# Performance work log

Hardware: AMD Instinct MI355X
Metric: run time of the kernel (lower is better)

## Reference

```python
import jax, jax.numpy as jnp
import numpy as np

EPS = 1e-8  # torch CosineSimilarity default eps

def _cosine(a, b):
    # cosine similarity along last dim, torch semantics: clamp norms to eps
    num = jnp.sum(a * b, axis=-1)
    na = jnp.maximum(jnp.linalg.norm(a, axis=-1), EPS)
    nb = jnp.maximum(jnp.linalg.norm(b, axis=-1), EPS)
    return num / (na * nb)

def setup_inputs() -> dict:
    key = jax.random.key(0)
    k1, k2, k3, k4, k5, k6 = jax.random.split(key, 6)
    B, D, NU, NS, K = 4096, 128, 100000, 50000, 5
    return {
        "user_embeddings": jax.random.normal(k1, (B, D), dtype=jnp.float32),
        "subreddit_embeddings": jax.random.normal(k2, (B, D), dtype=jnp.float32),
        "total_user_embeddings": jax.random.normal(k3, (NU, D), dtype=jnp.float32),
        "total_subreddit_embeddings": jax.random.normal(k4, (NS, D), dtype=jnp.float32),
        "batch_users": jax.random.randint(k5, (B,), 0, NU, dtype=jnp.int64) if jax.config.jax_enable_x64 else jax.random.randint(k5, (B,), 0, NU, dtype=jnp.int32),
        "neg_indices": jax.random.randint(k6, (B, K), 0, NS, dtype=jnp.int64) if jax.config.jax_enable_x64 else jax.random.randint(k6, (B, K), 0, NS, dtype=jnp.int32),
    }

def reference(user_embeddings, subreddit_embeddings, total_user_embeddings,
              total_subreddit_embeddings, batch_users, neg_indices):
    # positive term: cosine over paired batch embeddings
    pos = _cosine(user_embeddings, subreddit_embeddings)            # [B]
    # negative term: gather user table rows and sampled negative subreddit rows
    u = total_user_embeddings[batch_users]                          # [B, D]
    neg_emb = total_subreddit_embeddings[neg_indices]               # [B, K, D]
    neg = _cosine(u[:, None, :], neg_emb)                           # [B, K]
    positive_loss = 1.0 - jnp.mean(pos)
    negative_loss = jnp.mean(jnp.mean(neg, axis=-1))                # mean per user, then over users
    return positive_loss + negative_loss
```

## Files before the change

### kernel.cpp

```cpp
#include <hip/hip_runtime.h>
#include <math.h>

#define EPS 1e-8f
#define D 128
#define K 5

__global__ __launch_bounds__(256) void simloss_partial(
    const float* __restrict__ ue,
    const float* __restrict__ se,
    const float* __restrict__ tu,
    const float* __restrict__ ts,
    const int*   __restrict__ busers,
    const int*   __restrict__ negidx,
    float* __restrict__ partials,
    int B)
{
    const int t   = threadIdx.x;
    const int tid = blockIdx.x * 256 + t;
    const int row = tid >> 4;
    const int r   = t & 15;

    float diff = 0.0f;
    if (row < B) {
        const int uidx = busers[row];
        int nidx[K];
        #pragma unroll
        for (int k = 0; k < K; ++k) nidx[k] = negidx[row * K + k];

        const float4* A = (const float4*)(ue + (size_t)row * D);
        const float4* Bv = (const float4*)(se + (size_t)row * D);
        const float4 a0 = A[r],  a1 = A[r + 16];
        const float4 b0 = Bv[r], b1 = Bv[r + 16];
        float dot = a0.x*b0.x + a0.y*b0.y + a0.z*b0.z + a0.w*b0.w
                  + a1.x*b1.x + a1.y*b1.y + a1.z*b1.z + a1.w*b1.w;
        float na  = a0.x*a0.x + a0.y*a0.y + a0.z*a0.z + a0.w*a0.w
                  + a1.x*a1.x + a1.y*a1.y + a1.z*a1.z + a1.w*a1.w;
        float nb  = b0.x*b0.x + b0.y*b0.y + b0.z*b0.z + b0.w*b0.w
                  + b1.x*b1.x + b1.y*b1.y + b1.z*b1.z + b1.w*b1.w;

        const float4* Cv = (const float4*)(tu + (size_t)uidx * D);
        const float4 c0 = Cv[r], c1 = Cv[r + 16];
        float nc = c0.x*c0.x + c0.y*c0.y + c0.z*c0.z + c0.w*c0.w
                 + c1.x*c1.x + c1.y*c1.y + c1.z*c1.z + c1.w*c1.w;

        float dk[K], nk[K];
        #pragma unroll
        for (int k = 0; k < K; ++k) {
            const float4* E = (const float4*)(ts + (size_t)nidx[k] * D);
            const float4 e0 = E[r], e1 = E[r + 16];
            dk[k] = c0.x*e0.x + c0.y*e0.y + c0.z*e0.z + c0.w*e0.w
                  + c1.x*e1.x + c1.y*e1.y + c1.z*e1.z + c1.w*e1.w;
            nk[k] = e0.x*e0.x + e0.y*e0.y + e0.z*e0.z + e0.w*e0.w
                  + e1.x*e1.x + e1.y*e1.y + e1.z*e1.z + e1.w*e1.w;
        }

        #pragma unroll
        for (int off = 8; off > 0; off >>= 1) {
            dot += __shfl_xor(dot, off);
            na  += __shfl_xor(na,  off);
            nb  += __shfl_xor(nb,  off);
            nc  += __shfl_xor(nc,  off);
            #pragma unroll
            for (int k = 0; k < K; ++k) {
                dk[k] += __shfl_xor(dk[k], off);
                nk[k] += __shfl_xor(nk[k], off);
            }
        }

        const float pos = dot * rsqrtf(fmaxf(na, EPS * EPS))
                              * rsqrtf(fmaxf(nb, EPS * EPS));
        const float rc  = rsqrtf(fmaxf(nc, EPS * EPS));
        float s = 0.0f;
        #pragma unroll
        for (int k = 0; k < K; ++k)
            s += dk[k] * rc * rsqrtf(fmaxf(nk[k], EPS * EPS));
        diff = s * (1.0f / K) - pos;
    }

    __shared__ float sp[16];
    if (r == 0) sp[t >> 4] = diff;
    __syncthreads();
    if (t == 0) {
        float bp = 0.0f;
        #pragma unroll
        for (int i = 0; i < 16; ++i) bp += sp[i];
        partials[blockIdx.x] = bp;
    }
}

__global__ __launch_bounds__(64) void simloss_final(
    const float* __restrict__ partials, float* __restrict__ out, float invB)
{
    const int t = threadIdx.x;
    const float4 v = ((const float4*)partials)[t];
    float s = v.x + v.y + v.z + v.w;
    #pragma unroll
    for (int off = 32; off > 0; off >>= 1) s += __shfl_xor(s, off);
    if (t == 0) out[0] = 1.0f + s * invB;
}

extern "C" void kernel_launch(void* const* d_in, const int* in_sizes, int n_in,
                              void* d_out, int out_size, void* d_ws, size_t ws_size,
                              hipStream_t stream) {
    const float* ue = (const float*)d_in[0];
    const float* se = (const float*)d_in[1];
    const float* tu = (const float*)d_in[2];
    const float* ts = (const float*)d_in[3];
    const int*   bu = (const int*)d_in[4];
    const int*   ni = (const int*)d_in[5];
    float* out = (float*)d_out;

    const int B = in_sizes[0] / D;
    const int nblk = (B * 16 + 255) / 256;
    float* partials = (float*)d_ws;

    simloss_partial<<<nblk, 256, 0, stream>>>(ue, se, tu, ts, bu, ni, partials, B);
    simloss_final<<<1, 64, 0, stream>>>(partials, out, 1.0f / (float)B);
}
```

Before: 11.19 us.

## Fuse final reduction into main kernel via hierarchical atomic last-block counters

Replaces the two-kernel reduction with a single kernel in which each block publishes its partial sum and increments a two-level set of padded atomic counters. The block that finishes last sums all partials and writes the output, removing the second launch and its launch gap. The counters live in workspace and are never reset; they rely on wrapping modular arithmetic to detect the last block across calls. That works only when the workspace is zeroed initially and nblk is exactly 256, and it adds atomic and fence traffic to every block.

```diff
diff --git a/kernel.cpp b/kernel.cpp
--- a/kernel.cpp
+++ b/kernel.cpp
@@ -4,19 +4,25 @@
 #define EPS 1e-8f
 #define D 128
 #define K 5
+#define NG 16
+#define CPAD 16
 
-__global__ __launch_bounds__(256) void simloss_partial(
+__global__ __launch_bounds__(256) void simloss_onepass(
     const float* __restrict__ ue,
     const float* __restrict__ se,
     const float* __restrict__ tu,
     const float* __restrict__ ts,
     const int*   __restrict__ busers,
     const int*   __restrict__ negidx,
-    float* __restrict__ partials,
-    int B)
+    float*       __restrict__ out,
+    float*       __restrict__ partials,
+    unsigned*    __restrict__ cnt1,
+    unsigned*    __restrict__ cnt2,
+    int B, float invB, int nblk)
 {
+    const int bid = blockIdx.x;
     const int t   = threadIdx.x;
-    const int tid = blockIdx.x * 256 + t;
+    const int tid = bid * 256 + t;
     const int row = tid >> 4;
     const int r   = t & 15;
 
@@ -27,7 +33,7 @@
         #pragma unroll
         for (int k = 0; k < K; ++k) nidx[k] = negidx[row * K + k];
 
-        const float4* A = (const float4*)(ue + (size_t)row * D);
+        const float4* A  = (const float4*)(ue + (size_t)row * D);
         const float4* Bv = (const float4*)(se + (size_t)row * D);
         const float4 a0 = A[r],  a1 = A[r + 16];
         const float4 b0 = Bv[r], b1 = Bv[r + 16];
@@ -78,25 +84,64 @@
     }
 
     __shared__ float sp[16];
+    __shared__ int win;
     if (r == 0) sp[t >> 4] = diff;
     __syncthreads();
+
     if (t == 0) {
         float bp = 0.0f;
         #pragma unroll
         for (int i = 0; i < 16; ++i) bp += sp[i];
-        partials[blockIdx.x] = bp;
+        __hip_atomic_store((unsigned*)&partials[bid],
+                           __builtin_bit_cast(unsigned, bp),
+                           __ATOMIC_RELAXED, __HIP_MEMORY_SCOPE_AGENT);
+        __threadfence();
+        const int g = bid & (NG - 1);
+        int w2 = 0;
+        const unsigned o1 = __hip_atomic_fetch_add(&cnt1[g * CPAD], 1u,
+                               __ATOMIC_ACQ_REL, __HIP_MEMORY_SCOPE_AGENT);
+        if (((o1 + 1u) & (unsigned)(nblk / NG - 1)) == 0u) {
+            const unsigned o2 = __hip_atomic_fetch_add(cnt2, 1u,
+                                   __ATOMIC_ACQ_REL, __HIP_MEMORY_SCOPE_AGENT);
+            w2 = (((o2 + 1u) & (NG - 1)) == 0u);
+        }
+        win = w2;
     }
+    __syncthreads();
+    if (!win) return;
+
+    __threadfence();
+    float s = 0.0f;
+    if (t < nblk) {
+        const unsigned u = __hip_atomic_load((unsigned*)&partials[t],
+                              __ATOMIC_RELAXED, __HIP_MEMORY_SCOPE_AGENT);
+        s = __builtin_bit_cast(float, u);
+    }
+    #pragma unroll
+    for (int off = 32; off > 0; off >>= 1) s += __shfl_xor(s, off);
+
+    __shared__ float lw[4];
+    const int lane = t & 63, wave = t >> 6;
+    if (lane == 0) lw[wave] = s;
+    __syncthreads();
+    if (t == 0)
+        out[0] = 1.0f + (lw[0] + lw[1] + lw[2] + lw[3]) * invB;
 }
 
-__global__ __launch_bounds__(64) void simloss_final(
-    const float* __restrict__ partials, float* __restrict__ out, float invB)
+__global__ __launch_bounds__(256) void simloss_final(
+    const float* __restrict__ partials, float* __restrict__ out,
+    int nblk, float invB)
 {
     const int t = threadIdx.x;
-    const float4 v = ((const float4*)partials)[t];
-    float s = v.x + v.y + v.z + v.w;
+    float s = 0.0f;
+    for (int i = t; i < nblk; i += 256) s += partials[i];
     #pragma unroll
     for (int off = 32; off > 0; off >>= 1) s += __shfl_xor(s, off);
-    if (t == 0) out[0] = 1.0f + s * invB;
+    __shared__ float lw[4];
+    const int lane = t & 63, wave = t >> 6;
+    if (lane == 0) lw[wave] = s;
+    __syncthreads();
+    if (t == 0) out[0] = 1.0f + (lw[0] + lw[1] + lw[2] + lw[3]) * invB;
 }
 
 extern "C" void kernel_launch(void* const* d_in, const int* in_sizes, int n_in,
@@ -112,8 +157,19 @@
 
     const int B = in_sizes[0] / D;
     const int nblk = (B * 16 + 255) / 256;
-    float* partials = (float*)d_ws;
 
-    simloss_partial<<<nblk, 256, 0, stream>>>(ue, se, tu, ts, bu, ni, partials, B);
-    simloss_final<<<1, 64, 0, stream>>>(partials, out, 1.0f / (float)B);
+    float*    partials = (float*)d_ws;
+    unsigned* cnt1     = (unsigned*)(partials + nblk);
+    unsigned* cnt2     = cnt1 + NG * CPAD;
+
+    if (nblk == 256) {
+        simloss_onepass<<<nblk, 256, 0, stream>>>(ue, se, tu, ts, bu, ni, out,
+                                                  partials, cnt1, cnt2,
+                                                  B, 1.0f / (float)B, nblk);
+    } else {
+        simloss_onepass<<<nblk, 256, 0, stream>>>(ue, se, tu, ts, bu, ni, out,
+                                                  partials, cnt1, cnt2,
+                                                  B, 1.0f / (float)B, nblk);
+        simloss_final<<<1, 256, 0, stream>>>(partials, out, nblk, 1.0f / (float)B);
+    }
 }
```

Result: slower. 16.76 us (+49.8%).

## Fuse partial and final reduction into one cooperative kernel with grid sync

Applied to the files above, without the earlier changes.

Merges the two-kernel reduction into a single cooperative launch. Each block publishes its partial sum with an atomic store, then a grid-wide sync lets block 0 sum the 256 partials and write the result. This removes the second kernel launch and its inter-kernel gap, but adds the cost of a grid barrier and the cooperative launch path, which may be more expensive than a normal launch.

```diff
diff --git a/kernel.cpp b/kernel.cpp
--- a/kernel.cpp
+++ b/kernel.cpp
@@ -1,22 +1,27 @@
 #include <hip/hip_runtime.h>
+#include <hip/hip_cooperative_groups.h>
 #include <math.h>
+
+namespace cg = cooperative_groups;
 
 #define EPS 1e-8f
 #define D 128
 #define K 5
 
-__global__ __launch_bounds__(256) void simloss_partial(
+__global__ __launch_bounds__(256) void simloss_coop(
     const float* __restrict__ ue,
     const float* __restrict__ se,
     const float* __restrict__ tu,
     const float* __restrict__ ts,
     const int*   __restrict__ busers,
     const int*   __restrict__ negidx,
-    float* __restrict__ partials,
-    int B)
+    float*       __restrict__ out,
+    float*       __restrict__ partials,
+    int B, float invB)
 {
+    const int bid = blockIdx.x;
     const int t   = threadIdx.x;
-    const int tid = blockIdx.x * 256 + t;
+    const int tid = bid * 256 + t;
     const int row = tid >> 4;
     const int r   = t & 15;
 
@@ -27,7 +32,7 @@
         #pragma unroll
         for (int k = 0; k < K; ++k) nidx[k] = negidx[row * K + k];
 
-        const float4* A = (const float4*)(ue + (size_t)row * D);
+        const float4* A  = (const float4*)(ue + (size_t)row * D);
         const float4* Bv = (const float4*)(se + (size_t)row * D);
         const float4 a0 = A[r],  a1 = A[r + 16];
         const float4 b0 = Bv[r], b1 = Bv[r + 16];
@@ -84,19 +89,30 @@
         float bp = 0.0f;
         #pragma unroll
         for (int i = 0; i < 16; ++i) bp += sp[i];
-        partials[blockIdx.x] = bp;
+        __hip_atomic_store((unsigned*)&partials[bid],
+                           __builtin_bit_cast(unsigned, bp),
+                           __ATOMIC_RELAXED, __HIP_MEMORY_SCOPE_AGENT);
     }
-}
 
-__global__ __launch_bounds__(64) void simloss_final(
-    const float* __restrict__ partials, float* __restrict__ out, float invB)
-{
-    const int t = threadIdx.x;
-    const float4 v = ((const float4*)partials)[t];
-    float s = v.x + v.y + v.z + v.w;
+    cg::this_grid().sync();
+
+    if (bid != 0) return;
+    const int nblk = (int)gridDim.x;
+    float s = 0.0f;
+    if (t < nblk) {
+        const unsigned u = __hip_atomic_load((unsigned*)&partials[t],
+                              __ATOMIC_RELAXED, __HIP_MEMORY_SCOPE_AGENT);
+        s = __builtin_bit_cast(float, u);
+    }
     #pragma unroll
     for (int off = 32; off > 0; off >>= 1) s += __shfl_xor(s, off);
-    if (t == 0) out[0] = 1.0f + s * invB;
+
+    __shared__ float lw[4];
+    const int lane = t & 63, wave = t >> 6;
+    if (lane == 0) lw[wave] = s;
+    __syncthreads();
+    if (t == 0)
+        out[0] = 1.0f + (lw[0] + lw[1] + lw[2] + lw[3]) * invB;
 }
 
 extern "C" void kernel_launch(void* const* d_in, const int* in_sizes, int n_in,
@@ -110,10 +126,12 @@
     const int*   ni = (const int*)d_in[5];
     float* out = (float*)d_out;
 
-    const int B = in_sizes[0] / D;
-    const int nblk = (B * 16 + 255) / 256;
+    int B = in_sizes[0] / D;
+    int nblk = (B * 16 + 255) / 256;
     float* partials = (float*)d_ws;
+    float invB = 1.0f / (float)B;
 
-    simloss_partial<<<nblk, 256, 0, stream>>>(ue, se, tu, ts, bu, ni, partials, B);
-    simloss_final<<<1, 64, 0, stream>>>(partials, out, 1.0f / (float)B);
+    void* args[] = { &ue, &se, &tu, &ts, &bu, &ni, &out, &partials, &B, &invB };
+    hipLaunchCooperativeKernel((const void*)simloss_coop,
+                               dim3(nblk), dim3(256), args, 0, stream);
 }
```

After: 42.74 us. 282% more time.
